# Kernel optimization log

Hardware: AMD Instinct MI355X
Metric: run time of the kernel (lower is better)

## Reference

```python
import jax, jax.numpy as jnp
import numpy as np

N = 262144   # nodes
H = 256      # hidden_dim
NH = 8       # num_heads
HD = H // NH # head_dim = 32
C = 100      # num_commits
L = 2        # transformer layers


def _layer_norm(x, g, b, eps=1e-5):
    mu = jnp.mean(x, axis=-1, keepdims=True)
    var = jnp.mean(jnp.square(x - mu), axis=-1, keepdims=True)
    return (x - mu) * jax.lax.rsqrt(var + eps) * g + b


def setup_inputs() -> dict:
    key = jax.random.key(0)
    ks = jax.random.split(key, 16)
    w = lambda k, shape: jax.random.normal(k, shape, jnp.float32) * 0.02
    inp = {
        "node_embeddings": jax.random.normal(ks[0], (N, H), jnp.float32),
        "commit_indices": jax.random.randint(ks[1], (N,), 0, C),
        "num_commits": C,
        "commit_queries": jax.random.normal(ks[2], (NH, HD), jnp.float32),
        "k_w": w(ks[3], (H, H)), "k_b": jnp.zeros(H, jnp.float32),
        "v_w": w(ks[4], (H, H)), "v_b": jnp.zeros(H, jnp.float32),
        "po_w": w(ks[5], (H, H)), "po_b": jnp.zeros(H, jnp.float32),
        "pn_g": jnp.ones(H, jnp.float32), "pn_b": jnp.zeros(H, jnp.float32),
        "t_in_w": w(ks[6], (L, 3 * H, H)), "t_in_b": jnp.zeros((L, 3 * H), jnp.float32),
        "t_out_w": w(ks[7], (L, H, H)), "t_out_b": jnp.zeros((L, H), jnp.float32),
        "t_ln1_g": jnp.ones((L, H), jnp.float32), "t_ln1_b": jnp.zeros((L, H), jnp.float32),
        "t_ff1_w": w(ks[8], (L, 4 * H, H)), "t_ff1_b": jnp.zeros((L, 4 * H), jnp.float32),
        "t_ff2_w": w(ks[9], (L, H, 4 * H)), "t_ff2_b": jnp.zeros((L, H), jnp.float32),
        "t_ln2_g": jnp.ones((L, H), jnp.float32), "t_ln2_b": jnp.zeros((L, H), jnp.float32),
        "r1_w": w(ks[10], (H // 2, H)), "r1_b": jnp.zeros(H // 2, jnp.float32),
        "r2_w": w(ks[11], (1, H // 2)), "r2_b": jnp.zeros(1, jnp.float32),
    }
    return inp


def reference(node_embeddings, commit_indices, num_commits, commit_queries,
              k_w, k_b, v_w, v_b, po_w, po_b, pn_g, pn_b,
              t_in_w, t_in_b, t_out_w, t_out_b, t_ln1_g, t_ln1_b,
              t_ff1_w, t_ff1_b, t_ff2_w, t_ff2_b, t_ln2_g, t_ln2_b,
              r1_w, r1_b, r2_w, r2_b):
    nh, hd = commit_queries.shape
    scale = hd ** -0.5
    n = node_embeddings.shape[0]
    seg = commit_indices

    # --- segmented multi-head attention pooling (replaces per-commit loop) ---
    K = (node_embeddings @ k_w.T + k_b).reshape(n, nh, hd)   # [N,H,D]
    V = (node_embeddings @ v_w.T + v_b).reshape(n, nh, hd)
    scores = jnp.einsum('hd,nhd->nh', commit_queries, K) * scale  # [N,H]
    m = jax.ops.segment_max(scores, seg, num_segments=num_commits)  # [C,H]
    m = jnp.where(jnp.isfinite(m), m, 0.0)                          # empty commits
    e = jnp.exp(scores - m[seg])                                    # [N,H]
    den = jax.ops.segment_sum(e, seg, num_segments=num_commits)     # [C,H]
    num = jax.ops.segment_sum(e[:, :, None] * V, seg, num_segments=num_commits)  # [C,H,D]
    pooled = num / jnp.where(den > 0, den, 1.0)[:, :, None]
    counts = jax.ops.segment_sum(jnp.ones((n,), node_embeddings.dtype), seg,
                                 num_segments=num_commits)
    emb = _layer_norm(pooled.reshape(num_commits, nh * hd) @ po_w.T + po_b, pn_g, pn_b)
    x = jnp.where((counts > 0)[:, None], emb, 0.0)                  # [C,hidden]

    # --- commit transformer (seq len = C, batch = 1, post-norm, gelu) ---
    for l in range(t_in_w.shape[0]):
        qkv = x @ t_in_w[l].T + t_in_b[l]
        q, k, v = jnp.split(qkv, 3, axis=-1)
        q = q.reshape(num_commits, nh, hd)
        k = k.reshape(num_commits, nh, hd)
        v = v.reshape(num_commits, nh, hd)
        a = jax.nn.softmax(jnp.einsum('nhd,mhd->hnm', q, k) * scale, axis=-1)
        o = jnp.einsum('hnm,mhd->nhd', a, v).reshape(num_commits, nh * hd)
        o = o @ t_out_w[l].T + t_out_b[l]
        x = _layer_norm(x + o, t_ln1_g[l], t_ln1_b[l])
        ff = jax.nn.gelu(x @ t_ff1_w[l].T + t_ff1_b[l], approximate=False)
        ff = ff @ t_ff2_w[l].T + t_ff2_b[l]
        x = _layer_norm(x + ff, t_ln2_g[l], t_ln2_b[l])

    # --- ranking head ---
    h = jax.nn.gelu(x @ r1_w.T + r1_b, approximate=False)
    return (h @ r2_w.T + r2_b).squeeze(-1)  # [C]
```

## Files before the change

kernel.cpp:

```cpp
#include <hip/hip_runtime.h>
#include <math.h>

#define NNODES 262144
#define HDIM   256
#define NHEADS 8
#define HEADD  32
#define NC     100
#define NLAYER 2
#define SPLIT  16
#define NBLK   (NNODES/256)

__device__ __forceinline__ float gelu_exact(float v) {
    return 0.5f * v * (1.0f + erff(v * 0.70710678118654752440f));
}

__device__ __forceinline__ float dot4(float4 a, float4 b) {
    return a.x*b.x + a.y*b.y + a.z*b.z + a.w*b.w;
}

__device__ __forceinline__ float blk_sum256(float v, float* red, int tid) {
    #pragma unroll
    for (int m = 32; m >= 1; m >>= 1) v += __shfl_xor(v, m, 64);
    if ((tid & 63) == 0) red[tid >> 6] = v;
    __syncthreads();
    float tot = red[0] + red[1] + red[2] + red[3];
    __syncthreads();
    return tot;
}

__global__ void k_qkw(const float* __restrict__ q, const float* __restrict__ kw,
                      const float* __restrict__ kb, float* __restrict__ qk_w,
                      float* __restrict__ qk_b) {
    int h = blockIdx.x, j = threadIdx.x;
    float s = 0.f;
    #pragma unroll
    for (int d = 0; d < HEADD; ++d) s += q[h*HEADD + d] * kw[(h*HEADD + d)*HDIM + j];
    qk_w[h*HDIM + j] = s;
    if (j == 0) {
        float sb = 0.f;
        #pragma unroll
        for (int d = 0; d < HEADD; ++d) sb += q[h*HEADD + d] * kb[h*HEADD + d];
        qk_b[h] = sb;
    }
}

__global__ __launch_bounds__(256, 6) void k_score(const float* __restrict__ emb,
        const float* __restrict__ qk_w, const float* __restrict__ qk_b,
        float* __restrict__ ev_out) {
    int tid = threadIdx.x, w = tid >> 6, lane = tid & 63;
    int s = lane & 7;
    int gw = blockIdx.x * 4 + w;
    int r0 = gw * 64;
    const float scale = 0.17677669529663688f;

    float4 w4[NHEADS];
    #pragma unroll
    for (int h = 0; h < NHEADS; ++h)
        w4[h] = ((const float4*)(qk_w + h*HDIM))[lane];
    float qkb_s = qk_b[s];

    const float4* base = (const float4*)(emb + (size_t)r0 * HDIM);
    float4 nxt = base[lane];
    float keep = 0.f;
    for (int r = 0; r < 64; ++r) {
        float4 cur = nxt;
        if (r < 63) nxt = base[(r + 1) * 64 + lane];
        float p[NHEADS];
        #pragma unroll
        for (int h = 0; h < NHEADS; ++h) p[h] = dot4(cur, w4[h]);
        float q0, q1, q2, q3;
        {
            bool sel = (s & 1) != 0;
            float a0 = __shfl_xor(p[0], 1, 64), a1 = __shfl_xor(p[1], 1, 64);
            q0 = sel ? (p[1] + a1) : (p[0] + a0);
            float a2 = __shfl_xor(p[2], 1, 64), a3 = __shfl_xor(p[3], 1, 64);
            q1 = sel ? (p[3] + a3) : (p[2] + a2);
            float a4 = __shfl_xor(p[4], 1, 64), a5 = __shfl_xor(p[5], 1, 64);
            q2 = sel ? (p[5] + a5) : (p[4] + a4);
            float a6 = __shfl_xor(p[6], 1, 64), a7 = __shfl_xor(p[7], 1, 64);
            q3 = sel ? (p[7] + a7) : (p[6] + a6);
        }
        float r0v, r1v;
        {
            bool sel = (s & 2) != 0;
            float b0 = __shfl_xor(q0, 2, 64), b1 = __shfl_xor(q1, 2, 64);
            r0v = sel ? (q1 + b1) : (q0 + b0);
            float b2 = __shfl_xor(q2, 2, 64), b3 = __shfl_xor(q3, 2, 64);
            r1v = sel ? (q3 + b3) : (q2 + b2);
        }
        float tt;
        {
            bool sel = (s & 4) != 0;
            float c0 = __shfl_xor(r0v, 4, 64), c1 = __shfl_xor(r1v, 4, 64);
            tt = sel ? (r1v + c1) : (r0v + c0);
        }
        tt += __shfl_xor(tt, 8, 64);
        tt += __shfl_xor(tt, 16, 64);
        tt += __shfl_xor(tt, 32, 64);
        float evv = __expf((tt + qkb_s) * scale);
        if ((lane >> 3) == (r & 7)) keep = evv;
        if ((r & 7) == 7)
            ev_out[(size_t)(r0 + r - 7) * NHEADS + lane] = keep;
    }
}

__global__ __launch_bounds__(256) void k_hist(const int* __restrict__ cidx,
                                              int* __restrict__ hist) {
    __shared__ int l_hist[NC];
    int tid = threadIdx.x;
    for (int i = tid; i < NC; i += 256) l_hist[i] = 0;
    __syncthreads();
    int c = cidx[blockIdx.x * 256 + tid];
    atomicAdd(&l_hist[c], 1);
    __syncthreads();
    for (int i = tid; i < NC; i += 256) hist[blockIdx.x*NC + i] = l_hist[i];
}

__global__ __launch_bounds__(256) void k_blockscan(const int* __restrict__ hist,
        int* __restrict__ bbase, int* __restrict__ counts) {
    int c = blockIdx.x, t = threadIdx.x;
    int v[4]; int loc = 0;
    #pragma unroll
    for (int i = 0; i < 4; ++i) { v[i] = hist[(t*4 + i)*NC + c]; loc += v[i]; }
    __shared__ int sc[256];
    sc[t] = loc; __syncthreads();
    for (int off = 1; off < 256; off <<= 1) {
        int x = (t >= off) ? sc[t - off] : 0;
        __syncthreads();
        sc[t] += x;
        __syncthreads();
    }
    int run = (t > 0) ? sc[t-1] : 0;
    #pragma unroll
    for (int i = 0; i < 4; ++i) { bbase[(t*4 + i)*NC + c] = run; run += v[i]; }
    if (t == 255) counts[c] = sc[255];
}

__global__ void k_scan(const int* __restrict__ counts, int* __restrict__ offs) {
    __shared__ int sc[128];
    int t = threadIdx.x;
    int v = (t < NC) ? counts[t] : 0;
    sc[t] = v; __syncthreads();
    for (int off = 1; off < 128; off <<= 1) {
        int x = (t >= off) ? sc[t - off] : 0;
        __syncthreads();
        sc[t] += x;
        __syncthreads();
    }
    if (t <= NC) offs[t] = sc[t] - v;
}

__global__ __launch_bounds__(256) void k_scatter(const int* __restrict__ cidx,
        const int* __restrict__ offs, const int* __restrict__ bbase,
        int* __restrict__ nlist) {
    __shared__ int sb[NC];
    __shared__ int lcur[NC];
    int t = threadIdx.x, blk = blockIdx.x;
    if (t < NC) { sb[t] = offs[t] + bbase[blk*NC + t]; lcur[t] = 0; }
    __syncthreads();
    int n = blk * 256 + t;
    int c = cidx[n];
    int p = atomicAdd(&lcur[c], 1);
    nlist[sb[c] + p] = n;
}

__global__ __launch_bounds__(256, 8) void k_accum(const float* __restrict__ emb,
        const float* __restrict__ ev, const int* __restrict__ nlist,
        const int* __restrict__ offs, const int* __restrict__ counts,
        float* __restrict__ S_part, float* __restrict__ den_part) {
    int c  = blockIdx.x / SPLIT;
    int sl = blockIdx.x % SPLIT;
    int cnt = counts[c];
    __shared__ float s_buf[2][NHEADS*HDIM];
    __shared__ float s_den[2][NHEADS];
    int tid = threadIdx.x, w = tid >> 6, lane = tid & 63;
    int s = lane & 7, i = lane >> 3;

    float4 acc[NHEADS];
    #pragma unroll
    for (int h = 0; h < NHEADS; ++h) acc[h] = make_float4(0.f, 0.f, 0.f, 0.f);
    float den_l = 0.f;

    int beg = offs[c];
    int per = (cnt + SPLIT - 1) / SPLIT;
    int s0 = min(cnt, sl * per), s1 = min(cnt, s0 + per);

    for (int base = s0 + w*8; base < s1; base += 32) {
        int nb = min(8, s1 - base);
        int nn = (i < nb) ? nlist[beg + base + i] : 0;
        int n2 = __shfl(nn, 0, 64);
        float4 e_n = ((const float4*)(emb + (size_t)n2 * HDIM))[lane];
        float  v_n = ev[(size_t)n2 * NHEADS + s];
        for (int i2 = 0; i2 < nb; ++i2) {
            float4 e_c = e_n;
            float  v_c = v_n;
            if (i2 + 1 < nb) {
                int nx = __shfl(nn, (i2 + 1) * 8, 64);
                e_n = ((const float4*)(emb + (size_t)nx * HDIM))[lane];
                v_n = ev[(size_t)nx * NHEADS + s];
            }
            den_l += v_c;
            #pragma unroll
            for (int h2 = 0; h2 < NHEADS; ++h2) {
                float ee = __shfl(v_c, h2, 8);
                acc[h2].x += ee * e_c.x; acc[h2].y += ee * e_c.y;
                acc[h2].z += ee * e_c.z; acc[h2].w += ee * e_c.w;
            }
        }
    }
    if (w >= 2) {
        #pragma unroll
        for (int h2 = 0; h2 < NHEADS; ++h2)
            ((float4*)&s_buf[w-2][h2*HDIM])[lane] = acc[h2];
        if (lane < NHEADS) s_den[w-2][lane] = den_l;
    }
    __syncthreads();
    if (w < 2) {
        #pragma unroll
        for (int h2 = 0; h2 < NHEADS; ++h2) {
            float4 v = ((const float4*)&s_buf[w][h2*HDIM])[lane];
            acc[h2].x += v.x; acc[h2].y += v.y; acc[h2].z += v.z; acc[h2].w += v.w;
        }
        if (lane < NHEADS) den_l += s_den[w][lane];
    }
    __syncthreads();
    if (w == 1) {
        #pragma unroll
        for (int h2 = 0; h2 < NHEADS; ++h2)
            ((float4*)&s_buf[0][h2*HDIM])[lane] = acc[h2];
        if (lane < NHEADS) s_den[0][lane] = den_l;
    }
    __syncthreads();
    if (w == 0) {
        float* Sd = S_part + ((size_t)sl*NC + c) * (NHEADS*HDIM);
        #pragma unroll
        for (int h2 = 0; h2 < NHEADS; ++h2) {
            float4 v = ((const float4*)&s_buf[0][h2*HDIM])[lane];
            v.x += acc[h2].x; v.y += acc[h2].y; v.z += acc[h2].z; v.w += acc[h2].w;
            ((float4*)(Sd + h2*HDIM))[lane] = v;
        }
        if (lane < NHEADS)
            den_part[(sl*NC + c)*NHEADS + lane] = den_l + s_den[0][lane];
    }
}

__global__ __launch_bounds__(256) void k_pool(const float* __restrict__ S_part,
        const float* __restrict__ den_part, const int* __restrict__ counts,
        const float* __restrict__ vw, const float* __restrict__ vb,
        const float* __restrict__ pow_, const float* __restrict__ pob,
        const float* __restrict__ png, const float* __restrict__ pnb,
        float* __restrict__ x) {
    int c = blockIdx.x, t = threadIdx.x;
    __shared__ float S_l[NHEADS*HDIM];
    __shared__ float pooled[HDIM];
    __shared__ float red[4];
    {
        float4 a0 = make_float4(0.f,0.f,0.f,0.f), a1 = a0;
        #pragma unroll
        for (int sl = 0; sl < SPLIT; ++sl) {
            const float4* sp = (const float4*)(S_part + ((size_t)sl*NC + c) * (NHEADS*HDIM));
            float4 v0 = sp[t], v1 = sp[t + 256];
            a0.x += v0.x; a0.y += v0.y; a0.z += v0.z; a0.w += v0.w;
            a1.x += v1.x; a1.y += v1.y; a1.z += v1.z; a1.w += v1.w;
        }
        ((float4*)S_l)[t] = a0;
        ((float4*)S_l)[t + 256] = a1;
    }
    int h = t >> 5;
    float dh = 0.f;
    #pragma unroll
    for (int sl = 0; sl < SPLIT; ++sl) dh += den_part[(sl*NC + c)*NHEADS + h];
    __syncthreads();
    float dx = dh > 0.f ? dh : 1.f;
    float s = vb[t] * dh;
    const float4* wr = (const float4*)(vw + (size_t)t * HDIM);
    const float4* sr = (const float4*)(S_l + h * HDIM);
    #pragma unroll 8
    for (int j = 0; j < HDIM/4; ++j) s += dot4(wr[j], sr[j]);
    pooled[t] = s / dx;
    __syncthreads();
    float o = pob[t];
    const float4* pr = (const float4*)(pow_ + (size_t)t * HDIM);
    const float4* pv = (const float4*)pooled;
    #pragma unroll 8
    for (int j = 0; j < HDIM/4; ++j) o += dot4(pr[j], pv[j]);
    float mu  = blk_sum256(o, red, t) * (1.f/256.f);
    float d   = o - mu;
    float var = blk_sum256(d*d, red, t) * (1.f/256.f);
    float y = d * rsqrtf(var + 1e-5f) * png[t] + pnb[t];
    x[c*HDIM + t] = (counts[c] > 0) ? y : 0.f;
}

__global__ __launch_bounds__(256) void k_mm(const float* __restrict__ in,
        const float* __restrict__ W, const float* __restrict__ bias,
        float* __restrict__ out, int K, int P, int do_gelu) {
    int r = blockIdx.x;
    int p = blockIdx.y * 256 + threadIdx.x;
    __shared__ float xr[1024];
    for (int idx = threadIdx.x; idx < K; idx += 256) xr[idx] = in[(size_t)r*K + idx];
    __syncthreads();
    float s = bias[p];
    const float4* wr = (const float4*)(W + (size_t)p * K);
    const float4* xv = (const float4*)xr;
    for (int j = 0; j < (K >> 2); ++j) s += dot4(wr[j], xv[j]);
    if (do_gelu) s = gelu_exact(s);
    out[(size_t)r*P + p] = s;
}

__global__ __launch_bounds__(256) void k_mm_res_ln(const float* __restrict__ in,
        const float* __restrict__ W, const float* __restrict__ bias,
        const float* __restrict__ g, const float* __restrict__ be,
        float* __restrict__ x, int K) {
    int r = blockIdx.x, t = threadIdx.x;
    __shared__ float xr[1024];
    __shared__ float red[4];
    for (int idx = t; idx < K; idx += 256) xr[idx] = in[(size_t)r*K + idx];
    __syncthreads();
    float s = bias[t];
    const float4* wr = (const float4*)(W + (size_t)t * K);
    const float4* xv = (const float4*)xr;
    for (int j = 0; j < (K >> 2); ++j) s += dot4(wr[j], xv[j]);
    float v = x[r*HDIM + t] + s;
    float mu  = blk_sum256(v, red, t) * (1.f/256.f);
    float d   = v - mu;
    float var = blk_sum256(d*d, red, t) * (1.f/256.f);
    x[r*HDIM + t] = d * rsqrtf(var + 1e-5f) * g[t] + be[t];
}

__global__ __launch_bounds__(256) void k_attn(const float* __restrict__ qkv,
        float* __restrict__ attn_out) {
    int h = blockIdx.x, t = threadIdx.x;
    __shared__ float k_l[NC * HEADD];
    __shared__ float sc[NC * NC];
    for (int idx = t; idx < NC*HEADD; idx += 256) {
        int n = idx >> 5, d = idx & 31;
        k_l[idx] = qkv[n*768 + 256 + h*HEADD + d];
    }
    __syncthreads();
    const float scale = 0.17677669529663688f;
    for (int idx = t; idx < NC*NC; idx += 256) {
        int n = idx / NC, m = idx - n*NC;
        const float4* q4 = (const float4*)(qkv + n*768 + h*HEADD);
        const float4* k4 = (const float4*)(k_l + m*HEADD);
        float s = 0.f;
        #pragma unroll
        for (int j = 0; j < HEADD/4; ++j) s += dot4(q4[j], k4[j]);
        sc[idx] = s * scale;
    }
    __syncthreads();
    if (t < NC) {
        float mx = -1e30f;
        for (int m = 0; m < NC; ++m) mx = fmaxf(mx, sc[t*NC + m]);
        float sum = 0.f;
        for (int m = 0; m < NC; ++m) { float e = expf(sc[t*NC + m] - mx); sc[t*NC + m] = e; sum += e; }
        float inv = 1.f / sum;
        for (int m = 0; m < NC; ++m) sc[t*NC + m] *= inv;
    }
    __syncthreads();
    for (int idx = t; idx < NC*HEADD; idx += 256) {
        int n = idx >> 5, d = idx & 31;
        float o = 0.f;
        for (int m = 0; m < NC; ++m) o += sc[n*NC + m] * qkv[m*768 + 512 + h*HEADD + d];
        attn_out[n*HDIM + h*HEADD + d] = o;
    }
}

__global__ __launch_bounds__(128) void k_head(const float* __restrict__ x,
        const float* __restrict__ r1w, const float* __restrict__ r1b,
        const float* __restrict__ r2w, const float* __restrict__ r2b,
        float* __restrict__ out) {
    int r = blockIdx.x, t = threadIdx.x;
    __shared__ float xr[HDIM];
    __shared__ float red[2];
    xr[t] = x[r*HDIM + t];
    xr[t + 128] = x[r*HDIM + t + 128];
    __syncthreads();
    float s = r1b[t];
    const float4* wr = (const float4*)(r1w + (size_t)t * HDIM);
    const float4* xv = (const float4*)xr;
    #pragma unroll 8
    for (int j = 0; j < HDIM/4; ++j) s += dot4(wr[j], xv[j]);
    s = gelu_exact(s);
    float contrib = s * r2w[t];
    #pragma unroll
    for (int m = 32; m >= 1; m >>= 1) contrib += __shfl_xor(contrib, m, 64);
    if ((t & 63) == 0) red[t >> 6] = contrib;
    __syncthreads();
    if (t == 0) out[r] = red[0] + red[1] + r2b[0];
}

extern "C" void kernel_launch(void* const* d_in, const int* in_sizes, int n_in,
                              void* d_out, int out_size, void* d_ws, size_t ws_size,
                              hipStream_t stream) {
    const float* emb   = (const float*)d_in[0];
    const int*   cidx  = (const int*)d_in[1];
    const float* q     = (const float*)d_in[3];
    const float* kw    = (const float*)d_in[4];
    const float* kb    = (const float*)d_in[5];
    const float* vw    = (const float*)d_in[6];
    const float* vb    = (const float*)d_in[7];
    const float* pow_  = (const float*)d_in[8];
    const float* pob   = (const float*)d_in[9];
    const float* png   = (const float*)d_in[10];
    const float* pnb   = (const float*)d_in[11];
    const float* tinw  = (const float*)d_in[12];
    const float* tinb  = (const float*)d_in[13];
    const float* toutw = (const float*)d_in[14];
    const float* toutb = (const float*)d_in[15];
    const float* ln1g  = (const float*)d_in[16];
    const float* ln1b  = (const float*)d_in[17];
    const float* ff1w  = (const float*)d_in[18];
    const float* ff1b  = (const float*)d_in[19];
    const float* ff2w  = (const float*)d_in[20];
    const float* ff2b  = (const float*)d_in[21];
    const float* ln2g  = (const float*)d_in[22];
    const float* ln2b  = (const float*)d_in[23];
    const float* r1w   = (const float*)d_in[24];
    const float* r1b   = (const float*)d_in[25];
    const float* r2w   = (const float*)d_in[26];
    const float* r2b   = (const float*)d_in[27];
    float* out = (float*)d_out;

    char* ws = (char*)d_ws;
    size_t off = 0;
    auto alloc = [&](size_t bytes) -> char* {
        off = (off + 255) & ~(size_t)255;
        char* p = ws + off;
        off += bytes;
        return p;
    };
    int*   hist   = (int*)alloc((size_t)NBLK * NC * 4);
    int*   bbase  = (int*)alloc((size_t)NBLK * NC * 4);
    int*   counts = (int*)alloc(NC * 4);
    int*   offs   = (int*)alloc((NC + 1) * 4);
    float* den_p  = (float*)alloc((size_t)SPLIT * NC * NHEADS * 4);
    float* S_part = (float*)alloc((size_t)SPLIT * NC * NHEADS * HDIM * 4);
    float* qk_w   = (float*)alloc(NHEADS * HDIM * 4);
    float* qk_b   = (float*)alloc(NHEADS * 4);
    int*   nlist  = (int*)alloc((size_t)NNODES * 4);
    float* x      = (float*)alloc(NC * HDIM * 4);
    float* qkv    = (float*)alloc(NC * 3 * HDIM * 4);
    float* attn_o = (float*)alloc(NC * HDIM * 4);
    float* ffb    = (float*)alloc(NC * 4 * HDIM * 4);
    float* ev     = (float*)alloc((size_t)NNODES * NHEADS * 4);
    (void)ws_size; (void)in_sizes; (void)n_in; (void)out_size;

    k_qkw<<<NHEADS, HDIM, 0, stream>>>(q, kw, kb, qk_w, qk_b);
    k_score<<<NBLK, 256, 0, stream>>>(emb, qk_w, qk_b, ev);
    k_hist<<<NBLK, 256, 0, stream>>>(cidx, hist);
    k_blockscan<<<NC, 256, 0, stream>>>(hist, bbase, counts);
    k_scan<<<1, 128, 0, stream>>>(counts, offs);
    k_scatter<<<NBLK, 256, 0, stream>>>(cidx, offs, bbase, nlist);
    k_accum<<<NC*SPLIT, 256, 0, stream>>>(emb, ev, nlist, offs, counts, S_part, den_p);
    k_pool<<<NC, 256, 0, stream>>>(S_part, den_p, counts, vw, vb, pow_, pob, png, pnb, x);

    for (int l = 0; l < NLAYER; ++l) {
        k_mm<<<dim3(NC, 3), 256, 0, stream>>>(x, tinw + (size_t)l*3*HDIM*HDIM,
                                              tinb + (size_t)l*3*HDIM, qkv, HDIM, 3*HDIM, 0);
        k_attn<<<NHEADS, 256, 0, stream>>>(qkv, attn_o);
        k_mm_res_ln<<<NC, 256, 0, stream>>>(attn_o, toutw + (size_t)l*HDIM*HDIM,
                                            toutb + (size_t)l*HDIM, ln1g + (size_t)l*HDIM,
                                            ln1b + (size_t)l*HDIM, x, HDIM);
        k_mm<<<dim3(NC, 4), 256, 0, stream>>>(x, ff1w + (size_t)l*4*HDIM*HDIM,
                                              ff1b + (size_t)l*4*HDIM, ffb, HDIM, 4*HDIM, 1);
        k_mm_res_ln<<<NC, 256, 0, stream>>>(ffb, ff2w + (size_t)l*HDIM*4*HDIM,
                                            ff2b + (size_t)l*HDIM, ln2g + (size_t)l*HDIM,
                                            ln2b + (size_t)l*HDIM, x, 4*HDIM);
    }
    k_head<<<NC, 128, 0, stream>>>(x, r1w, r1b, r2w, r2b, out);
}
```

Before: 785.0 us.

## Double-buffer row loads in score and accumulate kernels, load ev as float4

The score kernel now issues two row loads ahead in an unrolled, ping-ponged loop so more memory requests are in flight. The accumulate kernel prefetches the next node-list chunk, double-buffers embedding rows, and loads all eight head weights as two float4 vectors instead of shuffling them across lanes. SPLIT drops from 16 to 15 and the occupancy hint goes from 8 to 6 blocks per CU. The aim is to cut gather latency and shuffle overhead, at the cost of more registers and lower occupancy.

After: 772.0 us. Within noise of the previous version (-1.7%).

```diff
diff --git a/kernel.cpp b/kernel.cpp
--- a/kernel.cpp
+++ b/kernel.cpp
@@ -7,7 +7,7 @@
 #define HEADD  32
 #define NC     100
 #define NLAYER 2
-#define SPLIT  16
+#define SPLIT  15
 #define NBLK   (NNODES/256)
 
 __device__ __forceinline__ float gelu_exact(float v) {
@@ -59,12 +59,10 @@
         w4[h] = ((const float4*)(qk_w + h*HDIM))[lane];
     float qkb_s = qk_b[s];
 
-    const float4* base = (const float4*)(emb + (size_t)r0 * HDIM);
-    float4 nxt = base[lane];
+    const float4* base4 = (const float4*)(emb + (size_t)r0 * HDIM);
     float keep = 0.f;
-    for (int r = 0; r < 64; ++r) {
-        float4 cur = nxt;
-        if (r < 63) nxt = base[(r + 1) * 64 + lane];
+
+    auto PROC = [&](float4 cur, int r) {
         float p[NHEADS];
         #pragma unroll
         for (int h = 0; h < NHEADS; ++h) p[h] = dot4(cur, w4[h]);
@@ -101,6 +99,15 @@
         if ((lane >> 3) == (r & 7)) keep = evv;
         if ((r & 7) == 7)
             ev_out[(size_t)(r0 + r - 7) * NHEADS + lane] = keep;
+    };
+
+    float4 eA = base4[lane];
+    #pragma unroll 4
+    for (int r = 0; r < 64; r += 2) {
+        float4 eB = base4[(r + 1) * 64 + lane];
+        PROC(eA, r);
+        if (r + 2 < 64) eA = base4[(r + 2) * 64 + lane];
+        PROC(eB, r + 1);
     }
 }
 
@@ -164,7 +171,7 @@
     nlist[sb[c] + p] = n;
 }
 
-__global__ __launch_bounds__(256, 8) void k_accum(const float* __restrict__ emb,
+__global__ __launch_bounds__(256, 6) void k_accum(const float* __restrict__ emb,
         const float* __restrict__ ev, const int* __restrict__ nlist,
         const int* __restrict__ offs, const int* __restrict__ counts,
         float* __restrict__ S_part, float* __restrict__ den_part) {
@@ -174,45 +181,84 @@
     __shared__ float s_buf[2][NHEADS*HDIM];
     __shared__ float s_den[2][NHEADS];
     int tid = threadIdx.x, w = tid >> 6, lane = tid & 63;
-    int s = lane & 7, i = lane >> 3;
+    int i = lane >> 3;
 
     float4 acc[NHEADS];
     #pragma unroll
     for (int h = 0; h < NHEADS; ++h) acc[h] = make_float4(0.f, 0.f, 0.f, 0.f);
-    float den_l = 0.f;
+    float4 den_a = make_float4(0.f, 0.f, 0.f, 0.f);
+    float4 den_b = make_float4(0.f, 0.f, 0.f, 0.f);
 
     int beg = offs[c];
     int per = (cnt + SPLIT - 1) / SPLIT;
     int s0 = min(cnt, sl * per), s1 = min(cnt, s0 + per);
 
-    for (int base = s0 + w*8; base < s1; base += 32) {
+#define ROWLOAD(nreg, e_, va_, vb_)                                          \
+    e_  = ((const float4*)(emb + (size_t)(nreg) * HDIM))[lane];              \
+    va_ = *(const float4*)(ev + (size_t)(nreg) * NHEADS);                    \
+    vb_ = *(const float4*)(ev + (size_t)(nreg) * NHEADS + 4);
+
+    int base = s0 + w*8;
+    int nn = 0;
+    if (base < s1) {
+        int nb0 = min(8, s1 - base);
+        if (i < nb0) nn = nlist[beg + base + i];
+    }
+    for (; base < s1; base += 32) {
         int nb = min(8, s1 - base);
-        int nn = (i < nb) ? nlist[beg + base + i] : 0;
-        int n2 = __shfl(nn, 0, 64);
-        float4 e_n = ((const float4*)(emb + (size_t)n2 * HDIM))[lane];
-        float  v_n = ev[(size_t)n2 * NHEADS + s];
-        for (int i2 = 0; i2 < nb; ++i2) {
-            float4 e_c = e_n;
-            float  v_c = v_n;
+        int nn_next = 0;
+        int base2 = base + 32;
+        if (base2 < s1) {
+            int nb2 = min(8, s1 - base2);
+            if (i < nb2) nn_next = nlist[beg + base2 + i];
+        }
+        float4 eA, eB, vaA, vbA, vaB, vbB;
+        int n0 = __shfl(nn, 0, 64);
+        ROWLOAD(n0, eA, vaA, vbA);
+        #pragma unroll
+        for (int i2 = 0; i2 < 8; ++i2) {
+            if (i2 >= nb) break;
             if (i2 + 1 < nb) {
                 int nx = __shfl(nn, (i2 + 1) * 8, 64);
-                e_n = ((const float4*)(emb + (size_t)nx * HDIM))[lane];
-                v_n = ev[(size_t)nx * NHEADS + s];
+                if ((i2 & 1) == 0) { ROWLOAD(nx, eB, vaB, vbB); }
+                else               { ROWLOAD(nx, eA, vaA, vbA); }
             }
-            den_l += v_c;
-            #pragma unroll
-            for (int h2 = 0; h2 < NHEADS; ++h2) {
-                float ee = __shfl(v_c, h2, 8);
-                acc[h2].x += ee * e_c.x; acc[h2].y += ee * e_c.y;
-                acc[h2].z += ee * e_c.z; acc[h2].w += ee * e_c.w;
-            }
-        }
-    }
+            float4 e_c  = (i2 & 1) ? eB  : eA;
+            float4 va_c = (i2 & 1) ? vaB : vaA;
+            float4 vb_c = (i2 & 1) ? vbB : vbA;
+            den_a.x += va_c.x; den_a.y += va_c.y; den_a.z += va_c.z; den_a.w += va_c.w;
+            den_b.x += vb_c.x; den_b.y += vb_c.y; den_b.z += vb_c.z; den_b.w += vb_c.w;
+            acc[0].x += va_c.x * e_c.x; acc[0].y += va_c.x * e_c.y;
+            acc[0].z += va_c.x * e_c.z; acc[0].w += va_c.x * e_c.w;
+            acc[1].x += va_c.y * e_c.x; acc[1].y += va_c.y * e_c.y;
+            acc[1].z += va_c.y * e_c.z; acc[1].w += va_c.y * e_c.w;
+            acc[2].x += va_c.z * e_c.x; acc[2].y += va_c.z * e_c.y;
+            acc[2].z += va_c.z * e_c.z; acc[2].w += va_c.z * e_c.w;
+            acc[3].x += va_c.w * e_c.x; acc[3].y += va_c.w * e_c.y;
+            acc[3].z += va_c.w * e_c.z; acc[3].w += va_c.w * e_c.w;
+            acc[4].x += vb_c.x * e_c.x; acc[4].y += vb_c.x * e_c.y;
+            acc[4].z += vb_c.x * e_c.z; acc[4].w += vb_c.x * e_c.w;
+            acc[5].x += vb_c.y * e_c.x; acc[5].y += vb_c.y * e_c.y;
+            acc[5].z += vb_c.y * e_c.z; acc[5].w += vb_c.y * e_c.w;
+            acc[6].x += vb_c.z * e_c.x; acc[6].y += vb_c.z * e_c.y;
+            acc[6].z += vb_c.z * e_c.z; acc[6].w += vb_c.z * e_c.w;
+            acc[7].x += vb_c.w * e_c.x; acc[7].y += vb_c.w * e_c.y;
+            acc[7].z += vb_c.w * e_c.z; acc[7].w += vb_c.w * e_c.w;
+        }
+        nn = nn_next;
+    }
+#undef ROWLOAD
+
     if (w >= 2) {
         #pragma unroll
         for (int h2 = 0; h2 < NHEADS; ++h2)
             ((float4*)&s_buf[w-2][h2*HDIM])[lane] = acc[h2];
-        if (lane < NHEADS) s_den[w-2][lane] = den_l;
+        if (lane == 0) {
+            s_den[w-2][0] = den_a.x; s_den[w-2][1] = den_a.y;
+            s_den[w-2][2] = den_a.z; s_den[w-2][3] = den_a.w;
+            s_den[w-2][4] = den_b.x; s_den[w-2][5] = den_b.y;
+            s_den[w-2][6] = den_b.z; s_den[w-2][7] = den_b.w;
+        }
     }
     __syncthreads();
     if (w < 2) {
@@ -221,14 +267,22 @@
             float4 v = ((const float4*)&s_buf[w][h2*HDIM])[lane];
             acc[h2].x += v.x; acc[h2].y += v.y; acc[h2].z += v.z; acc[h2].w += v.w;
         }
-        if (lane < NHEADS) den_l += s_den[w][lane];
+        den_a.x += s_den[w][0]; den_a.y += s_den[w][1];
+        den_a.z += s_den[w][2]; den_a.w += s_den[w][3];
+        den_b.x += s_den[w][4]; den_b.y += s_den[w][5];
+        den_b.z += s_den[w][6]; den_b.w += s_den[w][7];
     }
     __syncthreads();
     if (w == 1) {
         #pragma unroll
         for (int h2 = 0; h2 < NHEADS; ++h2)
             ((float4*)&s_buf[0][h2*HDIM])[lane] = acc[h2];
-        if (lane < NHEADS) s_den[0][lane] = den_l;
+        if (lane == 0) {
+            s_den[0][0] = den_a.x; s_den[0][1] = den_a.y;
+            s_den[0][2] = den_a.z; s_den[0][3] = den_a.w;
+            s_den[0][4] = den_b.x; s_den[0][5] = den_b.y;
+            s_den[0][6] = den_b.z; s_den[0][7] = den_b.w;
+        }
     }
     __syncthreads();
     if (w == 0) {
@@ -239,8 +293,13 @@
             v.x += acc[h2].x; v.y += acc[h2].y; v.z += acc[h2].z; v.w += acc[h2].w;
             ((float4*)(Sd + h2*HDIM))[lane] = v;
         }
-        if (lane < NHEADS)
-            den_part[(sl*NC + c)*NHEADS + lane] = den_l + s_den[0][lane];
+        if (lane == 0) {
+            float* dp = den_part + ((size_t)sl*NC + c) * NHEADS;
+            dp[0] = den_a.x + s_den[0][0]; dp[1] = den_a.y + s_den[0][1];
+            dp[2] = den_a.z + s_den[0][2]; dp[3] = den_a.w + s_den[0][3];
+            dp[4] = den_b.x + s_den[0][4]; dp[5] = den_b.y + s_den[0][5];
+            dp[6] = den_b.z + s_den[0][6]; dp[7] = den_b.w + s_den[0][7];
+        }
     }
 }
 
```
